# Performance work log

Measured on AMD Instinct MI355X. Metric: run time of the kernel, lower is better.

## Reference

```python
import jax, jax.numpy as jnp
import numpy as np

QMIN, QMAX = 0.0, 255.0  # uint8 activation quantization range


def _qlinear(x, w_q, b, s_in, zp_in, s_w):
    """zentorch_qlinear: quantize fp32 x to uint8, int8 weight, dequant output.

    x:   [M, K] fp32
    w_q: [N, K] int8 values (stored int32), symmetric (weight zp = 0)
    b:   [N] fp32
    s_in, zp_in: scalars (activation scale / zero point)
    s_w: [N] per-output-channel weight scales
    """
    zp = zp_in.astype(jnp.float32)
    q = jnp.clip(jnp.round(x / s_in) + zp, QMIN, QMAX)      # fake-quant uint8
    x_dq = (q - zp) * s_in                                   # dequantized activation
    w_dq = w_q.astype(jnp.float32) * s_w[:, None]            # [N, K] dequant weight
    return x_dq @ w_dq.T + b                                 # [M, N] fp32


def setup_inputs() -> dict:
    key = jax.random.key(0)
    k1, k2, k3, k4 = jax.random.split(key, 4)
    M, K, N = 8192, 4096, 4096
    inp = {
        "input": jax.random.normal(k1, (M, K), dtype=jnp.float32),
        "weights": jax.random.randint(k2, (N, K), -128, 128, dtype=jnp.int32),
        "biases": jax.random.normal(k3, (N,), dtype=jnp.float32) * 0.1,
        "input_scales": jnp.array([0.05], dtype=jnp.float32),
        "input_zero_points": jnp.array([128], dtype=jnp.int32),
        "weight_scales": jax.random.uniform(k4, (N,), dtype=jnp.float32, minval=0.001, maxval=0.01),
        "weight_zero_points": jnp.zeros((N,), dtype=jnp.int32),
        "output_dtype": 0,  # 0 -> float32
    }
    return inp


def reference(input, weights, biases, input_scales, input_zero_points,
              weight_scales, weight_zero_points, output_dtype):
    s_in = input_scales[0]
    zp_in = input_zero_points[0]
    x = _qlinear(input, weights, biases, s_in, zp_in, weight_scales)
    x = _qlinear(x, weights, biases, s_in, zp_in, weight_scales)
    x = _qlinear(x, weights, biases, s_in, zp_in, weight_scales)
    return x
```

## Files before the change

kernel.cpp:

```cpp
#include <hip/hip_runtime.h>
#include <stdint.h>

#define M_DIM 8192
#define K_DIM 4096
#define N_DIM 4096
#define KTILES (K_DIM / 64)

typedef __attribute__((ext_vector_type(4))) int i32x4;

__global__ void pack_w_kernel(const int* __restrict__ w, char* __restrict__ wp,
                              int* __restrict__ corr, const int* __restrict__ zpp) {
  __shared__ int red[256];
  const int n = blockIdx.x;
  const int t = threadIdx.x;
  const int4* row = (const int4*)(w + (size_t)n * K_DIM);
  int s = 0;
  int words[4];
#pragma unroll
  for (int u = 0; u < 4; ++u) {
    int4 v = row[t * 4 + u];
    s += v.x + v.y + v.z + v.w;
    words[u] = (v.x & 255) | ((v.y & 255) << 8) | ((v.z & 255) << 16) | (v.w << 24);
  }
  ((int4*)(wp + (size_t)n * K_DIM))[t] = make_int4(words[0], words[1], words[2], words[3]);
  red[t] = s;
  __syncthreads();
  for (int off = 128; off > 0; off >>= 1) {
    if (t < off) red[t] += red[t + off];
    __syncthreads();
  }
  if (t == 0) corr[n] = (128 - zpp[0]) * red[0];
}

__global__ void quant_in_kernel(const float* __restrict__ x, char* __restrict__ q,
                                const float* __restrict__ sp, const int* __restrict__ zpp) {
  const int i = blockIdx.x * blockDim.x + threadIdx.x;
  const float s = sp[0];
  const float zp = (float)zpp[0];
  float4 v = ((const float4*)x)[i];
  float t0 = fminf(fmaxf(rintf(v.x / s) + zp, 0.f), 255.f);
  float t1 = fminf(fmaxf(rintf(v.y / s) + zp, 0.f), 255.f);
  float t2 = fminf(fmaxf(rintf(v.z / s) + zp, 0.f), 255.f);
  float t3 = fminf(fmaxf(rintf(v.w / s) + zp, 0.f), 255.f);
  int b0 = (int)t0 - 128, b1 = (int)t1 - 128, b2 = (int)t2 - 128, b3 = (int)t3 - 128;
  ((int*)q)[i] = (b0 & 255) | ((b1 & 255) << 8) | ((b2 & 255) << 16) | (b3 << 24);
}

#define VM8 asm volatile("s_waitcnt vmcnt(8)" ::: "memory")
#define VM4 asm volatile("s_waitcnt vmcnt(4)" ::: "memory")
#define VM0 asm volatile("s_waitcnt vmcnt(0)" ::: "memory")
#define VMN ((void)0)

#define GEMM_TILE(T, DO_STAGE, VM_A)                                                   \
  {                                                                                    \
    const int buf_ = (T) & 3;                                                          \
    const int nslot_ = ((T) + 3) & 3;                                                  \
    char* bufA_ = &lds[buf_][0][0];                                                    \
    char* bufB_ = &lds[buf_][1][0];                                                    \
    i32x4 af[4], bf[4];                                                                \
    _Pragma("unroll") for (int i = 0; i < 4; ++i)                                      \
        af[i] = *(const i32x4*)(bufA_ + aoff[i]);                                      \
    _Pragma("unroll") for (int j = 0; j < 4; ++j)                                      \
        bf[j] = *(const i32x4*)(bufB_ + boff[j]);                                      \
    if (DO_STAGE) {                                                                    \
      STAGE16(asrc0 + (size_t)((T) + 3) * 64, &lds[nslot_][0][o0_]);                   \
      STAGE16(asrc1 + (size_t)((T) + 3) * 64, &lds[nslot_][0][o1_]);                   \
    }                                                                                  \
    __builtin_amdgcn_s_barrier();                                                      \
    asm volatile("s_waitcnt lgkmcnt(0)" ::: "memory");                                 \
    __builtin_amdgcn_s_setprio(1);                                                     \
    _Pragma("unroll") for (int i = 0; i < 4; ++i)                                      \
        _Pragma("unroll") for (int j = 0; j < 4; ++j)                                  \
            acc[i][j] = __builtin_amdgcn_mfma_i32_16x16x64_i8(af[i], bf[j], acc[i][j], 0, 0, 0); \
    __builtin_amdgcn_s_setprio(0);                                                     \
    __builtin_amdgcn_s_barrier();                                                      \
    i32x4 af2[4];                                                                      \
    _Pragma("unroll") for (int i = 0; i < 4; ++i)                                      \
        af2[i] = *(const i32x4*)(bufA_ + aoff[4 + i]);                                 \
    if (DO_STAGE) {                                                                    \
      STAGE16(bsrc0 + (size_t)((T) + 3) * 64, &lds[nslot_][1][o0_]);                   \
      STAGE16(bsrc1 + (size_t)((T) + 3) * 64, &lds[nslot_][1][o1_]);                   \
    }                                                                                  \
    VM_A;                                                                              \
    __builtin_amdgcn_s_barrier();                                                      \
    asm volatile("s_waitcnt lgkmcnt(0)" ::: "memory");                                 \
    __builtin_amdgcn_s_setprio(1);                                                     \
    _Pragma("unroll") for (int i = 0; i < 4; ++i)                                      \
        _Pragma("unroll") for (int j = 0; j < 4; ++j)                                  \
            acc[4 + i][j] = __builtin_amdgcn_mfma_i32_16x16x64_i8(af2[i], bf[j], acc[4 + i][j], 0, 0, 0); \
    __builtin_amdgcn_s_setprio(0);                                                     \
    __builtin_amdgcn_s_barrier();                                                      \
  }

#define STAGE16(SRC, DST)                                                              \
  __builtin_amdgcn_global_load_lds(                                                    \
      (const __attribute__((address_space(1))) void*)(SRC),                            \
      (__attribute__((address_space(3))) void*)(DST), 16, 0, 0)

template <int WRITE_Q>
__global__ __launch_bounds__(512, 2) void gemm_kernel(
    const char* __restrict__ qa, const char* __restrict__ wb,
    const int* __restrict__ corr, const float* __restrict__ swp,
    const float* __restrict__ bias, const float* __restrict__ sp,
    const int* __restrict__ zpp, char* __restrict__ outq, float* __restrict__ outf) {
  __shared__ __align__(16) char lds[4][2][256 * 64];
  const int tid = threadIdx.x;
  const int lane = tid & 63;
  const int w = tid >> 6;
  const int wr = w >> 2;
  const int wc = w & 3;
  const int bid = blockIdx.x;
  const int bm = bid & 31;
  const int bn = bid >> 5;
  const char* abase = qa + (size_t)bm * 256 * K_DIM;
  const char* bbase = wb + (size_t)bn * 256 * K_DIM;

  const int o0_ = tid * 16;
  const int o1_ = 8192 + tid * 16;
  const int r0_ = o0_ >> 6, r1_ = o1_ >> 6;
  const int g0_ = ((o0_ >> 4) & 3) ^ ((r0_ >> 1) & 3);
  const int g1_ = ((o1_ >> 4) & 3) ^ ((r1_ >> 1) & 3);
  const char* asrc0 = abase + (size_t)r0_ * K_DIM + g0_ * 16;
  const char* asrc1 = abase + (size_t)r1_ * K_DIM + g1_ * 16;
  const char* bsrc0 = bbase + (size_t)r0_ * K_DIM + g0_ * 16;
  const char* bsrc1 = bbase + (size_t)r1_ * K_DIM + g1_ * 16;

  const int rr = lane & 15;
  const int g = lane >> 4;
  int aoff[8], boff[4];
#pragma unroll
  for (int i = 0; i < 8; ++i) {
    const int row = wr * 128 + i * 16 + rr;
    aoff[i] = (row << 6) + ((g ^ ((row >> 1) & 3)) << 4);
  }
#pragma unroll
  for (int j = 0; j < 4; ++j) {
    const int row = wc * 64 + j * 16 + rr;
    boff[j] = (row << 6) + ((g ^ ((row >> 1) & 3)) << 4);
  }

  i32x4 acc[8][4] = {};

  STAGE16(asrc0, &lds[0][0][o0_]); STAGE16(asrc1, &lds[0][0][o1_]);
  STAGE16(bsrc0, &lds[0][1][o0_]); STAGE16(bsrc1, &lds[0][1][o1_]);
  STAGE16(asrc0 + 64, &lds[1][0][o0_]); STAGE16(asrc1 + 64, &lds[1][0][o1_]);
  STAGE16(bsrc0 + 64, &lds[1][1][o0_]); STAGE16(bsrc1 + 64, &lds[1][1][o1_]);
  STAGE16(asrc0 + 128, &lds[2][0][o0_]); STAGE16(asrc1 + 128, &lds[2][0][o1_]);
  STAGE16(bsrc0 + 128, &lds[2][1][o0_]); STAGE16(bsrc1 + 128, &lds[2][1][o1_]);
  asm volatile("s_waitcnt vmcnt(8)" ::: "memory");
  __builtin_amdgcn_s_barrier();

  for (int t = 0; t < KTILES - 3; ++t) GEMM_TILE(t, true, VM8);
  GEMM_TILE(KTILES - 3, false, VM4);
  GEMM_TILE(KTILES - 2, false, VM0);
  GEMM_TILE(KTILES - 1, false, VMN);

  const float s = sp[0];
  const float zpf = (float)zpp[0];
  const int m0 = bm * 256 + wr * 128 + (lane >> 4) * 4;
  const int n0 = bn * 256 + wc * 64 + (lane & 15);
#pragma unroll
  for (int j = 0; j < 4; ++j) {
    const int n = n0 + j * 16;
    const int cr = corr[n];
    const float fs = s * swp[n];
    const float bb = bias[n];
#pragma unroll
    for (int i = 0; i < 8; ++i) {
#pragma unroll
      for (int q = 0; q < 4; ++q) {
        const int m = m0 + i * 16 + q;
        float val = fs * (float)(acc[i][j][q] + cr) + bb;
        if (WRITE_Q) {
          float tq = fminf(fmaxf(rintf(val / s) + zpf, 0.f), 255.f);
          outq[(size_t)m * N_DIM + n] = (char)((int)tq - 128);
        } else {
          outf[(size_t)m * N_DIM + n] = val;
        }
      }
    }
  }
}

extern "C" void kernel_launch(void* const* d_in, const int* in_sizes, int n_in,
                              void* d_out, int out_size, void* d_ws, size_t ws_size,
                              hipStream_t stream) {
  const float* x = (const float*)d_in[0];
  const int* wq = (const int*)d_in[1];
  const float* bias = (const float*)d_in[2];
  const float* s_in = (const float*)d_in[3];
  const int* zp_in = (const int*)d_in[4];
  const float* s_w = (const float*)d_in[5];
  float* out = (float*)d_out;

  const size_t WP_BYTES = (size_t)N_DIM * K_DIM;
  const size_t Q_BYTES = (size_t)M_DIM * K_DIM;
  char* ws = (char*)d_ws;
  char* wp = ws;
  char* q1 = ws + WP_BYTES;
  char* q2 = q1 + Q_BYTES;
  int* corr = (int*)(q2 + Q_BYTES);
  const size_t NEEDED = WP_BYTES + 2 * Q_BYTES + (size_t)N_DIM * sizeof(int);
  if (ws_size < NEEDED) return;

  pack_w_kernel<<<N_DIM, 256, 0, stream>>>(wq, wp, corr, zp_in);
  quant_in_kernel<<<(M_DIM * K_DIM / 4) / 256, 256, 0, stream>>>(x, q1, s_in, zp_in);

  dim3 grid((M_DIM / 256) * (N_DIM / 256));
  dim3 blk(512);
  gemm_kernel<1><<<grid, blk, 0, stream>>>(q1, wp, corr, s_w, bias, s_in, zp_in, q2, nullptr);
  gemm_kernel<1><<<grid, blk, 0, stream>>>(q2, wp, corr, s_w, bias, s_in, zp_in, q1, nullptr);
  gemm_kernel<0><<<grid, blk, 0, stream>>>(q1, wp, corr, s_w, bias, s_in, zp_in, nullptr, out);
}
```

Before: 458.7 us.

## Software-pipeline LDS fragment reads and cut barriers in int8 GEMM main loop

Restructures the GEMM K-loop so the next tile's A/B register fragments are read from LDS while the current tile's MFMAs run. Per-tile synchronization drops from four barriers to one, with a single vmcnt wait. The loop is unrolled by four so the LDS ring-slot indices are compile-time constants. The tail iterations issue redundant re-stages of the last K tile instead of branching, which costs extra global loads and more live registers.

```diff
diff --git a/kernel.cpp b/kernel.cpp
--- a/kernel.cpp
+++ b/kernel.cpp
@@ -46,56 +46,53 @@
   ((int*)q)[i] = (b0 & 255) | ((b1 & 255) << 8) | ((b2 & 255) << 16) | (b3 << 24);
 }
 
-#define VM8 asm volatile("s_waitcnt vmcnt(8)" ::: "memory")
-#define VM4 asm volatile("s_waitcnt vmcnt(4)" ::: "memory")
-#define VM0 asm volatile("s_waitcnt vmcnt(0)" ::: "memory")
-#define VMN ((void)0)
-
-#define GEMM_TILE(T, DO_STAGE, VM_A)                                                   \
-  {                                                                                    \
-    const int buf_ = (T) & 3;                                                          \
-    const int nslot_ = ((T) + 3) & 3;                                                  \
-    char* bufA_ = &lds[buf_][0][0];                                                    \
-    char* bufB_ = &lds[buf_][1][0];                                                    \
-    i32x4 af[4], bf[4];                                                                \
-    _Pragma("unroll") for (int i = 0; i < 4; ++i)                                      \
-        af[i] = *(const i32x4*)(bufA_ + aoff[i]);                                      \
-    _Pragma("unroll") for (int j = 0; j < 4; ++j)                                      \
-        bf[j] = *(const i32x4*)(bufB_ + boff[j]);                                      \
-    if (DO_STAGE) {                                                                    \
-      STAGE16(asrc0 + (size_t)((T) + 3) * 64, &lds[nslot_][0][o0_]);                   \
-      STAGE16(asrc1 + (size_t)((T) + 3) * 64, &lds[nslot_][0][o1_]);                   \
-    }                                                                                  \
-    __builtin_amdgcn_s_barrier();                                                      \
-    asm volatile("s_waitcnt lgkmcnt(0)" ::: "memory");                                 \
-    __builtin_amdgcn_s_setprio(1);                                                     \
-    _Pragma("unroll") for (int i = 0; i < 4; ++i)                                      \
-        _Pragma("unroll") for (int j = 0; j < 4; ++j)                                  \
-            acc[i][j] = __builtin_amdgcn_mfma_i32_16x16x64_i8(af[i], bf[j], acc[i][j], 0, 0, 0); \
-    __builtin_amdgcn_s_setprio(0);                                                     \
-    __builtin_amdgcn_s_barrier();                                                      \
-    i32x4 af2[4];                                                                      \
-    _Pragma("unroll") for (int i = 0; i < 4; ++i)                                      \
-        af2[i] = *(const i32x4*)(bufA_ + aoff[4 + i]);                                 \
-    if (DO_STAGE) {                                                                    \
-      STAGE16(bsrc0 + (size_t)((T) + 3) * 64, &lds[nslot_][1][o0_]);                   \
-      STAGE16(bsrc1 + (size_t)((T) + 3) * 64, &lds[nslot_][1][o1_]);                   \
-    }                                                                                  \
-    VM_A;                                                                              \
-    __builtin_amdgcn_s_barrier();                                                      \
-    asm volatile("s_waitcnt lgkmcnt(0)" ::: "memory");                                 \
-    __builtin_amdgcn_s_setprio(1);                                                     \
-    _Pragma("unroll") for (int i = 0; i < 4; ++i)                                      \
-        _Pragma("unroll") for (int j = 0; j < 4; ++j)                                  \
-            acc[4 + i][j] = __builtin_amdgcn_mfma_i32_16x16x64_i8(af2[i], bf[j], acc[4 + i][j], 0, 0, 0); \
-    __builtin_amdgcn_s_setprio(0);                                                     \
-    __builtin_amdgcn_s_barrier();                                                      \
-  }
-
-#define STAGE16(SRC, DST)                                                              \
-  __builtin_amdgcn_global_load_lds(                                                    \
-      (const __attribute__((address_space(1))) void*)(SRC),                            \
+#define STAGE16(SRC, DST)                                                     \
+  __builtin_amdgcn_global_load_lds(                                           \
+      (const __attribute__((address_space(1))) void*)(SRC),                   \
       (__attribute__((address_space(3))) void*)(DST), 16, 0, 0)
+
+#define RD(p) (*(const i32x4*)(p))
+
+#define TILE(SLOT, KSTG, DO_NEXT)                                             \
+  {                                                                           \
+    const char* bufA_ = &lds[SLOT][0][0];                                     \
+    char* nA_ = &lds[((SLOT) + 3) & 3][0][0];                                 \
+    char* nB_ = &lds[((SLOT) + 3) & 3][1][0];                                 \
+    i32x4 a1_[4];                                                             \
+    _Pragma("unroll") for (int i_ = 0; i_ < 4; ++i_)                          \
+        a1_[i_] = RD(bufA_ + aoff[4 + i_]);                                   \
+    STAGE16(asrc0 + (size_t)(KSTG) * 64, nA_ + o0_);                          \
+    STAGE16(asrc1 + (size_t)(KSTG) * 64, nA_ + o1_);                          \
+    __builtin_amdgcn_s_setprio(1);                                            \
+    _Pragma("unroll") for (int i_ = 0; i_ < 4; ++i_)                          \
+        _Pragma("unroll") for (int j_ = 0; j_ < 4; ++j_)                      \
+            acc[i_][j_] = __builtin_amdgcn_mfma_i32_16x16x64_i8(              \
+                a0[i_], b0[j_], acc[i_][j_], 0, 0, 0);                        \
+    __builtin_amdgcn_s_setprio(0);                                            \
+    i32x4 ta_[4], tb_[4];                                                     \
+    if (DO_NEXT) {                                                            \
+      const char* xA_ = &lds[((SLOT) + 1) & 3][0][0];                         \
+      const char* xB_ = &lds[((SLOT) + 1) & 3][1][0];                         \
+      _Pragma("unroll") for (int i_ = 0; i_ < 4; ++i_)                        \
+          ta_[i_] = RD(xA_ + aoff[i_]);                                       \
+      _Pragma("unroll") for (int j_ = 0; j_ < 4; ++j_)                        \
+          tb_[j_] = RD(xB_ + boff[j_]);                                       \
+    }                                                                         \
+    STAGE16(bsrc0 + (size_t)(KSTG) * 64, nB_ + o0_);                          \
+    STAGE16(bsrc1 + (size_t)(KSTG) * 64, nB_ + o1_);                          \
+    __builtin_amdgcn_s_setprio(1);                                            \
+    _Pragma("unroll") for (int i_ = 0; i_ < 4; ++i_)                          \
+        _Pragma("unroll") for (int j_ = 0; j_ < 4; ++j_)                      \
+            acc[4 + i_][j_] = __builtin_amdgcn_mfma_i32_16x16x64_i8(          \
+                a1_[i_], b0[j_], acc[4 + i_][j_], 0, 0, 0);                   \
+    __builtin_amdgcn_s_setprio(0);                                            \
+    asm volatile("s_waitcnt vmcnt(4)" ::: "memory");                          \
+    __builtin_amdgcn_s_barrier();                                             \
+    if (DO_NEXT) {                                                            \
+      _Pragma("unroll") for (int i_ = 0; i_ < 4; ++i_) a0[i_] = ta_[i_];      \
+      _Pragma("unroll") for (int j_ = 0; j_ < 4; ++j_) b0[j_] = tb_[j_];      \
+    }                                                                         \
+  }
 
 template <int WRITE_Q>
 __global__ __launch_bounds__(512, 2) void gemm_kernel(
@@ -103,7 +100,7 @@
     const int* __restrict__ corr, const float* __restrict__ swp,
     const float* __restrict__ bias, const float* __restrict__ sp,
     const int* __restrict__ zpp, char* __restrict__ outq, float* __restrict__ outf) {
-  __shared__ __align__(16) char lds[4][2][256 * 64];
+  __shared__ __align__(16) char lds[4][2][16384];
   const int tid = threadIdx.x;
   const int lane = tid & 63;
   const int w = tid >> 6;
@@ -147,13 +144,27 @@
   STAGE16(bsrc0 + 64, &lds[1][1][o0_]); STAGE16(bsrc1 + 64, &lds[1][1][o1_]);
   STAGE16(asrc0 + 128, &lds[2][0][o0_]); STAGE16(asrc1 + 128, &lds[2][0][o1_]);
   STAGE16(bsrc0 + 128, &lds[2][1][o0_]); STAGE16(bsrc1 + 128, &lds[2][1][o1_]);
-  asm volatile("s_waitcnt vmcnt(8)" ::: "memory");
+  asm volatile("s_waitcnt vmcnt(4)" ::: "memory");
   __builtin_amdgcn_s_barrier();
 
-  for (int t = 0; t < KTILES - 3; ++t) GEMM_TILE(t, true, VM8);
-  GEMM_TILE(KTILES - 3, false, VM4);
-  GEMM_TILE(KTILES - 2, false, VM0);
-  GEMM_TILE(KTILES - 1, false, VMN);
+  i32x4 a0[4], b0[4];
+#pragma unroll
+  for (int i = 0; i < 4; ++i) a0[i] = RD(&lds[0][0][0] + aoff[i]);
+#pragma unroll
+  for (int j = 0; j < 4; ++j) b0[j] = RD(&lds[0][1][0] + boff[j]);
+
+  for (int tb = 0; tb < (KTILES - 4) / 4; ++tb) {
+    const int t0 = tb * 4;
+#pragma unroll
+    for (int u = 0; u < 4; ++u) {
+      TILE(u, t0 + u + 3, 1);
+    }
+  }
+  TILE(0, KTILES - 1, 1);
+  TILE(1, KTILES - 1, 1);
+  TILE(2, KTILES - 1, 1);
+  TILE(3, KTILES - 1, 0);
+  asm volatile("s_waitcnt vmcnt(0)" ::: "memory");
 
   const float s = sp[0];
   const float zpf = (float)zpp[0];
```

New measurement: 451.7 us. No clear change (-1.5%).
